# Kernel optimization log

Hardware: AMD Instinct MI355X
Metric: run time of the kernel (lower is better)

Reference implementation:

```python
import jax, jax.numpy as jnp
import numpy as np

B, C, N = 8, 512, 4096
G = 8          # GroupNorm groups (8 <= C)
EPS = 1e-6


def setup_inputs() -> dict:
    key = jax.random.key(0)
    ks = jax.random.split(key, 5)
    return {
        "x": jax.random.normal(ks[0], (B, C, N), dtype=jnp.float32),
        "qkv_w": jax.random.normal(ks[1], (3 * C, C), dtype=jnp.float32) * (C ** -0.5),
        "qkv_b": jax.random.normal(ks[2], (3 * C,), dtype=jnp.float32) * 0.02,
        "proj_w": jax.random.normal(ks[3], (C, C), dtype=jnp.float32) * (C ** -0.5),
        "proj_b": jax.random.normal(ks[4], (C,), dtype=jnp.float32) * 0.02,
        "gn_scale": jnp.ones((C,), dtype=jnp.float32),
        "gn_bias": jnp.zeros((C,), dtype=jnp.float32),
    }


def group_norm(x, scale, bias):
    b, c, n = x.shape
    xr = x.reshape(b, G, c // G, n)
    mean = xr.mean(axis=(2, 3), keepdims=True)
    var = xr.var(axis=(2, 3), keepdims=True)
    h = ((xr - mean) * jax.lax.rsqrt(var + EPS)).reshape(b, c, n)
    return h * scale[None, :, None] + bias[None, :, None]


def reference(x, qkv_w, qkv_b, proj_w, proj_b, gn_scale, gn_bias):
    c = x.shape[1]
    h = group_norm(x, gn_scale, gn_bias)
    # 1x1 Conv1d == channel-mixing GEMM
    qkv = jnp.einsum('oc,bcn->bon', qkv_w, h) + qkv_b[None, :, None]
    q, k, v = jnp.split(qkv, 3, axis=1)           # each [B, C, N]
    q = q * (c ** -0.5)
    k = jax.nn.softmax(k, axis=-1)                # softmax over tokens
    # linear attention: context = k v^T over tokens, then project q
    context = jnp.einsum('bdn,ben->bde', k, v)    # [B, C, C]
    out = jnp.einsum('bde,bdn->ben', context, q)  # [B, C, N]
    y = jnp.einsum('oc,bcn->bon', proj_w, out) + proj_b[None, :, None]
    return x + y
```

## Files before the change

kernel.cpp:

```cpp
#include <hip/hip_runtime.h>

#define BB 8
#define CC 512
#define NT 4096
#define GG 8
#define CPG 64
#define EPSF 1e-6f
#define SQK 0.04419417382415922f

typedef __attribute__((ext_vector_type(8))) short bf16x8;
typedef __attribute__((ext_vector_type(4))) float f32x4;

#define OFF_RED  0
#define OFF_PB2  4096
#define OFF_IZ   270336
#define OFF_WKV  274432
#define OFF_PWB  536576
#define OFF_WQT  667648
#define OFF_MB   798720
#define OFF_PBF  1847296
#define OFF_CTXB 2895872
#define OFF_PCTX 3944448
#define OFF_HT   12333056
#define OFF_KVB  20721664

__device__ __forceinline__ ushort f2bf(float f) {
  union { float f; uint u; } v; v.f = f;
  uint r = (v.u + 0x7fffu + ((v.u >> 16) & 1u)) >> 16;
  return (ushort)r;
}
__device__ __forceinline__ float bf2f(ushort h) {
  union { uint u; float f; } v; v.u = ((uint)h) << 16;
  return v.f;
}
__device__ __forceinline__ uint pk(float a, float b) {
  return (uint)f2bf(a) | ((uint)f2bf(b) << 16);
}
__device__ __forceinline__ void gload16(const ushort* g, ushort* l) {
  __builtin_amdgcn_global_load_lds((const __attribute__((address_space(1))) void*)g,
                                   (__attribute__((address_space(3))) void*)l, 16, 0, 0);
}
#define KSWZ(kofs, row) ((kofs) ^ ((((row) >> 1) & 3) << 3))

__global__ __launch_bounds__(256) void gn_stats1(const float* __restrict__ x,
                                                 float* __restrict__ red) {
  int bg = blockIdx.y, chunk = blockIdx.x;
  const float4* p4 = (const float4*)(x + (size_t)bg * (CPG * NT) + (size_t)chunk * 32768);
  int tid = threadIdx.x;
  float s = 0.f, sq = 0.f;
  for (int i = tid; i < 8192; i += 256) {
    float4 v = p4[i];
    s  += v.x + v.y + v.z + v.w;
    sq += v.x * v.x + v.y * v.y + v.z * v.z + v.w * v.w;
  }
  for (int off = 32; off > 0; off >>= 1) {
    s  += __shfl_down(s, off);
    sq += __shfl_down(sq, off);
  }
  __shared__ float ls[4], lq[4];
  int wid = tid >> 6, lane = tid & 63;
  if (lane == 0) { ls[wid] = s; lq[wid] = sq; }
  __syncthreads();
  if (tid == 0) {
    red[(bg * 8 + chunk) * 2]     = ls[0] + ls[1] + ls[2] + ls[3];
    red[(bg * 8 + chunk) * 2 + 1] = lq[0] + lq[1] + lq[2] + lq[3];
  }
}

__global__ __launch_bounds__(256) void wconv2(const float* __restrict__ qkv_w,
                                              const float* __restrict__ proj_w,
                                              ushort* __restrict__ wkvb,
                                              ushort* __restrict__ pwb) {
  int bid = blockIdx.x;
  if (bid < 512) {
    int idx = (bid * 256 + threadIdx.x) * 4;
    float4 v = *(const float4*)(qkv_w + (size_t)CC * CC + idx);
    *(uint2*)(wkvb + idx) = make_uint2(pk(v.x, v.y), pk(v.z, v.w));
  } else {
    int idx = ((bid - 512) * 256 + threadIdx.x) * 4;
    float4 v = *(const float4*)(proj_w + idx);
    *(uint2*)(pwb + idx) = make_uint2(pk(v.x, v.y), pk(v.z, v.w));
  }
}

__global__ __launch_bounds__(256) void wqt_kernel(const float* __restrict__ qkv_w,
                                                  ushort* __restrict__ wqT) {
  __shared__ float t[32][33];
  int d0 = blockIdx.y * 32, c0 = blockIdx.x * 32;
  int tid = threadIdx.x;
  int r = tid >> 3, c4 = (tid & 7) * 4;
  float4 v = *(const float4*)(qkv_w + (size_t)(d0 + r) * CC + c0 + c4);
  t[r][c4] = v.x; t[r][c4 + 1] = v.y; t[r][c4 + 2] = v.z; t[r][c4 + 3] = v.w;
  __syncthreads();
  int r2 = tid >> 3, d4 = (tid & 7) * 4;
  uint w0 = pk(t[d4][r2], t[d4 + 1][r2]);
  uint w1 = pk(t[d4 + 2][r2], t[d4 + 3][r2]);
  *(uint2*)&wqT[(size_t)(c0 + r2) * CC + d0 + d4] = make_uint2(w0, w1);
}

__global__ __launch_bounds__(256) void ht_kernel(
    const float* __restrict__ x, const float* __restrict__ red,
    const float* __restrict__ gn_scale, const float* __restrict__ gn_bias,
    ushort* __restrict__ hT) {
  __shared__ float ts[64][68];
  __shared__ float la[64], lb[64];
  int b = blockIdx.z, g = blockIdx.y, n0 = blockIdx.x * 64;
  int c0 = g * 64;
  int tid = threadIdx.x;
  if (tid == 0) {
    int bg = b * 8 + g;
    float s = 0.f, sq = 0.f;
#pragma unroll
    for (int i = 0; i < 8; i++) {
      s  += red[(bg * 8 + i) * 2];
      sq += red[(bg * 8 + i) * 2 + 1];
    }
    float mean = s / (float)(CPG * NT);
    float var  = sq / (float)(CPG * NT) - mean * mean;
    ts[0][0] = mean; ts[0][1] = rsqrtf(var + EPSF);
  }
  __syncthreads();
  if (tid < 64) {
    float mean = ts[0][0], rstd = ts[0][1];
    float a = gn_scale[c0 + tid] * rstd;
    la[tid] = a;
    lb[tid] = gn_bias[c0 + tid] - mean * a;
  }
  __syncthreads();
  int tn = (tid & 15) * 4, tc = tid >> 4;
#pragma unroll
  for (int it = 0; it < 4; it++) {
    int c = tc + it * 16;
    float a  = la[c];
    float bb = lb[c];
    float4 v = *(const float4*)(x + ((size_t)(b * CC + c0 + c)) * NT + n0 + tn);
    ts[c][tn]     = a * v.x + bb;
    ts[c][tn + 1] = a * v.y + bb;
    ts[c][tn + 2] = a * v.z + bb;
    ts[c][tn + 3] = a * v.w + bb;
  }
  __syncthreads();
#pragma unroll
  for (int it = 0; it < 2; it++) {
    int idx = tid + it * 256;
    int n = idx >> 3, c8 = (idx & 7) * 8;
    uint w[4];
#pragma unroll
    for (int j = 0; j < 4; j++)
      w[j] = pk(ts[c8 + 2 * j][n], ts[c8 + 2 * j + 1][n]);
    *(uint4*)&hT[((size_t)b * NT + n0 + n) * CC + c0 + c8] = make_uint4(w[0], w[1], w[2], w[3]);
  }
}

template <int KTOT, int LDA, int LDB>
__device__ __forceinline__ void mfma_loop(const ushort* __restrict__ A,
                                          const ushort* __restrict__ B,
                                          ushort* As, ushort* Bs, int tid,
                                          f32x4 acc[4][4]) {
  int wave = tid >> 6, lane = tid & 63;
  int srow = lane >> 2;
  int kofs = KSWZ((lane & 3) * 8, srow);
  int r0 = wave * 16 + srow;
  int r1 = (wave + 4) * 16 + srow;
  const ushort* ga0 = A + (size_t)r0 * LDA + kofs;
  const ushort* ga1 = A + (size_t)r1 * LDA + kofs;
  const ushort* gb0 = B + (size_t)r0 * LDB + kofs;
  const ushort* gb1 = B + (size_t)r1 * LDB + kofs;
  int lo0 = wave * 512, lo1 = (wave + 4) * 512;
  int wm = (wave >> 1) * 64, wn = (wave & 1) * 64;
  int rowl = lane & 15;
  int kread = KSWZ((lane >> 4) * 8, rowl);
  int aoff = (wm + rowl) * 32 + kread;
  int boff = (wn + rowl) * 32 + kread;
  constexpr int NIT = KTOT / 32;
  gload16(ga0, As + lo0); gload16(ga1, As + lo1);
  gload16(gb0, Bs + lo0); gload16(gb1, Bs + lo1);
  ga0 += 32; ga1 += 32; gb0 += 32; gb1 += 32;
#pragma unroll 1
  for (int t = 0; t < NIT; t++) {
    int cb = (t & 1) * 4096;
    int nb = 4096 - cb;
    if (t + 1 < NIT) {
      gload16(ga0, As + nb + lo0); gload16(ga1, As + nb + lo1);
      gload16(gb0, Bs + nb + lo0); gload16(gb1, Bs + nb + lo1);
      ga0 += 32; ga1 += 32; gb0 += 32; gb1 += 32;
      asm volatile("s_waitcnt vmcnt(4)" ::: "memory");
    } else {
      asm volatile("s_waitcnt vmcnt(0)" ::: "memory");
    }
    __builtin_amdgcn_s_barrier();
    asm volatile("" ::: "memory");
    bf16x8 a[4], b[4];
#pragma unroll
    for (int m = 0; m < 4; m++) a[m] = *(const bf16x8*)(As + cb + aoff + m * 512);
#pragma unroll
    for (int n = 0; n < 4; n++) b[n] = *(const bf16x8*)(Bs + cb + boff + n * 512);
#pragma unroll
    for (int m = 0; m < 4; m++)
#pragma unroll
      for (int n = 0; n < 4; n++)
        acc[m][n] = __builtin_amdgcn_mfma_f32_16x16x32_bf16(a[m], b[n], acc[m][n], 0, 0, 0);
    asm volatile("" ::: "memory");
    __builtin_amdgcn_s_barrier();
    asm volatile("" ::: "memory");
  }
}

template <int KTOT, int LDA, int LDB>
__device__ __forceinline__ void mfma_loop64(const ushort* __restrict__ A,
                                            const ushort* __restrict__ B,
                                            ushort* As, ushort* Bs, int tid,
                                            f32x4 acc[2][2]) {
  int wave = tid >> 6, lane = tid & 63;
  int srow = tid >> 2;
  int kofs = KSWZ((tid & 3) * 8, srow & 15);
  const ushort* ga = A + (size_t)srow * LDA + kofs;
  const ushort* gb = B + (size_t)srow * LDB + kofs;
  int lo = wave * 512;
  int wm = (wave >> 1) * 32, wn = (wave & 1) * 32;
  int rowl = lane & 15;
  int kread = KSWZ((lane >> 4) * 8, rowl);
  int aoff = (wm + rowl) * 32 + kread;
  int boff = (wn + rowl) * 32 + kread;
  constexpr int NIT = KTOT / 32;
  gload16(ga, As + lo); gload16(gb, Bs + lo);
  ga += 32; gb += 32;
#pragma unroll 1
  for (int t = 0; t < NIT; t++) {
    int cb = (t & 1) * 2048;
    int nb = 2048 - cb;
    if (t + 1 < NIT) {
      gload16(ga, As + nb + lo); gload16(gb, Bs + nb + lo);
      ga += 32; gb += 32;
      asm volatile("s_waitcnt vmcnt(2)" ::: "memory");
    } else {
      asm volatile("s_waitcnt vmcnt(0)" ::: "memory");
    }
    __builtin_amdgcn_s_barrier();
    asm volatile("" ::: "memory");
    bf16x8 a[2], b[2];
#pragma unroll
    for (int m = 0; m < 2; m++) a[m] = *(const bf16x8*)(As + cb + aoff + m * 512);
#pragma unroll
    for (int n = 0; n < 2; n++) b[n] = *(const bf16x8*)(Bs + cb + boff + n * 512);
#pragma unroll
    for (int m = 0; m < 2; m++)
#pragma unroll
      for (int n = 0; n < 2; n++)
        acc[m][n] = __builtin_amdgcn_mfma_f32_16x16x32_bf16(a[m], b[n], acc[m][n], 0, 0, 0);
    asm volatile("" ::: "memory");
    __builtin_amdgcn_s_barrier();
    asm volatile("" ::: "memory");
  }
}

__global__ __launch_bounds__(256) void kv_gemm_bf16(
    const ushort* __restrict__ wkvb, const ushort* __restrict__ hT,
    const float* __restrict__ qkv_b, ushort* __restrict__ kvb) {
  __shared__ ushort As[8192], Bs[8192];
  int b = blockIdx.z, n0 = blockIdx.x * 128, m0 = blockIdx.y * 128;
  int tid = threadIdx.x;
  f32x4 acc[4][4] = {{{0.f, 0.f, 0.f, 0.f}}};
  mfma_loop<CC, CC, CC>(wkvb + (size_t)m0 * CC,
                        hT + (size_t)b * NT * CC + (size_t)n0 * CC, As, Bs, tid, acc);
  int wave = tid >> 6, lane = tid & 63;
  int wm = (wave >> 1) * 64, wn = (wave & 1) * 64;
  int col = lane & 15, rb = (lane >> 4) * 4;
  bool isK = (m0 < 512);
#pragma unroll
  for (int m = 0; m < 4; m++)
#pragma unroll
    for (int n = 0; n < 4; n++)
#pragma unroll
      for (int j = 0; j < 4; j++) {
        int gm = m0 + wm + m * 16 + rb + j;
        int gn = n0 + wn + n * 16 + col;
        float val = acc[m][n][j] + qkv_b[CC + gm];
        if (isK) val = __expf(val);
        kvb[((size_t)(b * 1024 + gm)) * NT + gn] = f2bf(val);
      }
}

__global__ __launch_bounds__(256) void zred(const ushort* __restrict__ kvb,
                                            float* __restrict__ invZ) {
  int row = blockIdx.x;
  int b = row >> 9, d = row & 511;
  const ushort* p = kvb + ((size_t)(b * 1024 + d)) * NT;
  int tid = threadIdx.x;
  uint4 r0 = *(const uint4*)(p + tid * 16);
  uint4 r1 = *(const uint4*)(p + tid * 16 + 8);
  uint w[8] = {r0.x, r0.y, r0.z, r0.w, r1.x, r1.y, r1.z, r1.w};
  float s = 0.f;
#pragma unroll
  for (int i = 0; i < 8; i++) {
    union { uint u; float f; } lo, hi;
    lo.u = w[i] << 16; hi.u = w[i] & 0xffff0000u;
    s += lo.f + hi.f;
  }
  for (int off = 32; off > 0; off >>= 1) s += __shfl_down(s, off);
  __shared__ float red[4];
  int wid = tid >> 6, lane = tid & 63;
  if (lane == 0) red[wid] = s;
  __syncthreads();
  if (tid == 0) invZ[row] = 1.f / (red[0] + red[1] + red[2] + red[3]);
}

__global__ __launch_bounds__(256) void ctx_gemm_split(
    const ushort* __restrict__ kvb, ushort* __restrict__ pctx) {
  __shared__ ushort As[8192], Bs[8192];
  int e0 = blockIdx.x * 128, d0 = blockIdx.y * 128;
  int bz = blockIdx.z, b = bz >> 3, s = bz & 7;
  int tid = threadIdx.x;
  f32x4 acc[4][4] = {{{0.f, 0.f, 0.f, 0.f}}};
  const ushort* K = kvb + (size_t)b * 1024 * NT + (size_t)d0 * NT + s * 512;
  const ushort* V = kvb + ((size_t)b * 1024 + 512) * NT + (size_t)e0 * NT + s * 512;
  mfma_loop<512, NT, NT>(K, V, As, Bs, tid, acc);
  int wave = tid >> 6, lane = tid & 63;
  int wm = (wave >> 1) * 64, wn = (wave & 1) * 64;
  int col = lane & 15, rb = (lane >> 4) * 4;
#pragma unroll
  for (int m = 0; m < 4; m++)
#pragma unroll
    for (int n = 0; n < 4; n++)
#pragma unroll
      for (int j = 0; j < 4; j++) {
        int gd = d0 + wm + m * 16 + rb + j;
        int ge = e0 + wn + n * 16 + col;
        pctx[((size_t)(b * 8 + s) * CC + gd) * CC + ge] = f2bf(acc[m][n][j]);
      }
}

__global__ __launch_bounds__(256) void ctx_red(const ushort* __restrict__ pctx,
                                               const float* __restrict__ invZ,
                                               ushort* __restrict__ ctxb) {
  int t = blockIdx.x * 256 + threadIdx.x;
  int b = t >> 15;
  int r = (t & 32767) * 8;
  int d = r >> 9;
  float iz = invZ[b * 512 + d];
  const ushort* base = pctx + (size_t)b * 8 * 262144 + r;
  float f[8] = {};
#pragma unroll
  for (int s = 0; s < 8; s++) {
    uint4 v = *(const uint4*)(base + (size_t)s * 262144);
    uint w[4] = {v.x, v.y, v.z, v.w};
#pragma unroll
    for (int j = 0; j < 4; j++) {
      union { uint u; float f; } lo, hi;
      lo.u = w[j] << 16; hi.u = w[j] & 0xffff0000u;
      f[2 * j] += lo.f; f[2 * j + 1] += hi.f;
    }
  }
  uint o[4];
#pragma unroll
  for (int j = 0; j < 4; j++) o[j] = pk(f[2 * j] * iz, f[2 * j + 1] * iz);
  *(uint4*)(ctxb + (size_t)b * 262144 + r) = make_uint4(o[0], o[1], o[2], o[3]);
}

__global__ __launch_bounds__(256) void m_gemm_bf16(
    const ushort* __restrict__ pwb, const ushort* __restrict__ ctxb,
    ushort* __restrict__ Mb) {
  __shared__ ushort As[4096], Bs[4096];
  int b = blockIdx.z, d0 = blockIdx.x * 64, o0 = blockIdx.y * 64;
  int tid = threadIdx.x;
  f32x4 acc[2][2] = {{{0.f, 0.f, 0.f, 0.f}}};
  mfma_loop64<CC, CC, CC>(pwb + (size_t)o0 * CC,
                          ctxb + (size_t)b * CC * CC + (size_t)d0 * CC, As, Bs, tid, acc);
  int wave = tid >> 6, lane = tid & 63;
  int wm = (wave >> 1) * 32, wn = (wave & 1) * 32;
  int col = lane & 15, rb = (lane >> 4) * 4;
#pragma unroll
  for (int m = 0; m < 2; m++)
#pragma unroll
    for (int n = 0; n < 2; n++)
#pragma unroll
      for (int j = 0; j < 4; j++) {
        int go = o0 + wm + m * 16 + rb + j;
        int gd = d0 + wn + n * 16 + col;
        Mb[((size_t)b * CC + go) * CC + gd] = f2bf(acc[m][n][j] * SQK);
      }
}

__global__ __launch_bounds__(256) void p_gemm_bf16(
    const ushort* __restrict__ Mb, const ushort* __restrict__ wqT,
    ushort* __restrict__ Pb) {
  __shared__ ushort As[4096], Bs[4096];
  int b = blockIdx.z, c0 = blockIdx.x * 64, o0 = blockIdx.y * 64;
  int tid = threadIdx.x;
  f32x4 acc[2][2] = {{{0.f, 0.f, 0.f, 0.f}}};
  mfma_loop64<CC, CC, CC>(Mb + (size_t)b * CC * CC + (size_t)o0 * CC,
                          wqT + (size_t)c0 * CC, As, Bs, tid, acc);
  int wave = tid >> 6, lane = tid & 63;
  int wm = (wave >> 1) * 32, wn = (wave & 1) * 32;
  int col = lane & 15, rb = (lane >> 4) * 4;
#pragma unroll
  for (int m = 0; m < 2; m++)
#pragma unroll
    for (int n = 0; n < 2; n++)
#pragma unroll
      for (int j = 0; j < 4; j++) {
        int go = o0 + wm + m * 16 + rb + j;
        int gc = c0 + wn + n * 16 + col;
        Pb[((size_t)b * CC + go) * CC + gc] = f2bf(acc[m][n][j]);
      }
}

__global__ __launch_bounds__(256) void pb2_kernel(
    const ushort* __restrict__ Mb, const float* __restrict__ qkv_b,
    const float* __restrict__ proj_b, float* __restrict__ pb2) {
  int b = blockIdx.x, og = blockIdx.y;
  int r = og * 64 + (threadIdx.x >> 2);
  int q = threadIdx.x & 3;
  const ushort* Mr = Mb + ((size_t)(b * CC + r)) * CC + q * 128;
  const float* bq = qkv_b + q * 128;
  float s = 0.f;
#pragma unroll
  for (int i = 0; i < 16; i++) {
    uint4 v = *(const uint4*)(Mr + i * 8);
    uint w[4] = {v.x, v.y, v.z, v.w};
#pragma unroll
    for (int j = 0; j < 4; j++) {
      union { uint u; float f; } lo, hi;
      lo.u = w[j] << 16; hi.u = w[j] & 0xffff0000u;
      s += lo.f * bq[i * 8 + 2 * j] + hi.f * bq[i * 8 + 2 * j + 1];
    }
  }
  s += __shfl_xor(s, 1);
  s += __shfl_xor(s, 2);
  if (q == 0) pb2[b * CC + r] = s + proj_b[r];
}

__global__ __launch_bounds__(256) void final_gemm_bf16(
    const float* __restrict__ x, const ushort* __restrict__ Pb,
    const ushort* __restrict__ hT, const float* __restrict__ pb2,
    float* __restrict__ out) {
  __shared__ ushort As[8192], Bs[8192];
  int b = blockIdx.z, n0 = blockIdx.x * 128, m0 = blockIdx.y * 128;
  int tid = threadIdx.x;
  f32x4 acc[4][4] = {{{0.f, 0.f, 0.f, 0.f}}};
  mfma_loop<CC, CC, CC>(Pb + (size_t)b * CC * CC + (size_t)m0 * CC,
                        hT + (size_t)b * NT * CC + (size_t)n0 * CC, As, Bs, tid, acc);
  int wave = tid >> 6, lane = tid & 63;
  int wm = (wave >> 1) * 64, wn = (wave & 1) * 64;
  int col = lane & 15, rb = (lane >> 4) * 4;
#pragma unroll
  for (int m = 0; m < 4; m++)
#pragma unroll
    for (int n = 0; n < 4; n++)
#pragma unroll
      for (int j = 0; j < 4; j++) {
        int gm = m0 + wm + m * 16 + rb + j;
        int gn = n0 + wn + n * 16 + col;
        size_t idx = ((size_t)(b * CC + gm)) * NT + gn;
        out[idx] = acc[m][n][j] + pb2[b * CC + gm] + x[idx];
      }
}

extern "C" void kernel_launch(void* const* d_in, const int* in_sizes, int n_in,
                              void* d_out, int out_size, void* d_ws, size_t ws_size,
                              hipStream_t stream) {
  const float* x        = (const float*)d_in[0];
  const float* qkv_w    = (const float*)d_in[1];
  const float* qkv_b    = (const float*)d_in[2];
  const float* proj_w   = (const float*)d_in[3];
  const float* proj_b   = (const float*)d_in[4];
  const float* gn_scale = (const float*)d_in[5];
  const float* gn_bias  = (const float*)d_in[6];
  float* out = (float*)d_out;
  float* ws  = (float*)d_ws;

  float*  red   = ws + OFF_RED;
  float*  pb2   = ws + OFF_PB2;
  float*  invZ  = ws + OFF_IZ;
  ushort* wkvb  = (ushort*)(ws + OFF_WKV);
  ushort* pwb   = (ushort*)(ws + OFF_PWB);
  ushort* wqT   = (ushort*)(ws + OFF_WQT);
  ushort* Mb    = (ushort*)(ws + OFF_MB);
  ushort* Pb    = (ushort*)(ws + OFF_PBF);
  ushort* ctxb  = (ushort*)(ws + OFF_CTXB);
  ushort* pctx  = (ushort*)(ws + OFF_PCTX);
  ushort* hT    = (ushort*)(ws + OFF_HT);
  ushort* kvb   = (ushort*)(ws + OFF_KVB);

  gn_stats1<<<dim3(8, 64), 256, 0, stream>>>(x, red);
  wconv2<<<768, 256, 0, stream>>>(qkv_w, proj_w, wkvb, pwb);
  wqt_kernel<<<dim3(16, 16), 256, 0, stream>>>(qkv_w, wqT);
  ht_kernel<<<dim3(64, 8, 8), 256, 0, stream>>>(x, red, gn_scale, gn_bias, hT);
  kv_gemm_bf16<<<dim3(32, 8, 8), 256, 0, stream>>>(wkvb, hT, qkv_b, kvb);
  zred<<<4096, 256, 0, stream>>>(kvb, invZ);
  ctx_gemm_split<<<dim3(4, 4, 64), 256, 0, stream>>>(kvb, pctx);
  ctx_red<<<1024, 256, 0, stream>>>(pctx, invZ, ctxb);
  m_gemm_bf16<<<dim3(8, 8, 8), 256, 0, stream>>>(pwb, ctxb, Mb);
  p_gemm_bf16<<<dim3(8, 8, 8), 256, 0, stream>>>(Mb, wqT, Pb);
  pb2_kernel<<<dim3(8, 8), 256, 0, stream>>>(Mb, qkv_b, proj_b, pb2);
  final_gemm_bf16<<<dim3(32, 4, 8), 256, 0, stream>>>(x, Pb, hT, pb2, out);
}
```

Measured before the change: 208.4 us.

## Enlarge big GEMM tiles to 256x256 with 512 threads and K=64 stages

```diff
diff --git a/kernel.cpp b/kernel.cpp
--- a/kernel.cpp
+++ b/kernel.cpp
@@ -152,57 +152,68 @@
   }
 }
 
-template <int KTOT, int LDA, int LDB>
-__device__ __forceinline__ void mfma_loop(const ushort* __restrict__ A,
-                                          const ushort* __restrict__ B,
-                                          ushort* As, ushort* Bs, int tid,
-                                          f32x4 acc[4][4]) {
-  int wave = tid >> 6, lane = tid & 63;
-  int srow = lane >> 2;
-  int kofs = KSWZ((lane & 3) * 8, srow);
-  int r0 = wave * 16 + srow;
-  int r1 = (wave + 4) * 16 + srow;
-  const ushort* ga0 = A + (size_t)r0 * LDA + kofs;
-  const ushort* ga1 = A + (size_t)r1 * LDA + kofs;
-  const ushort* gb0 = B + (size_t)r0 * LDB + kofs;
-  const ushort* gb1 = B + (size_t)r1 * LDB + kofs;
-  int lo0 = wave * 512, lo1 = (wave + 4) * 512;
-  int wm = (wave >> 1) * 64, wn = (wave & 1) * 64;
-  int rowl = lane & 15;
-  int kread = KSWZ((lane >> 4) * 8, rowl);
-  int aoff = (wm + rowl) * 32 + kread;
-  int boff = (wn + rowl) * 32 + kread;
-  constexpr int NIT = KTOT / 32;
-  gload16(ga0, As + lo0); gload16(ga1, As + lo1);
-  gload16(gb0, Bs + lo0); gload16(gb1, Bs + lo1);
-  ga0 += 32; ga1 += 32; gb0 += 32; gb1 += 32;
+#define TBUF 16384
+
+__device__ __forceinline__ void stage256(const ushort* __restrict__ G, ushort* L,
+                                         int LD, int wave, int lane) {
+  int rw = wave * 8 + (lane >> 3);
+  int cg = lane & 7;
+#pragma unroll
+  for (int s = 0; s < 4; s++) {
+    int row = s * 64 + rw;
+    int gcol = (cg ^ (row & 7)) * 8;
+    gload16(G + (size_t)row * LD + gcol, L + s * 4096 + wave * 512);
+  }
+}
+
+template <int NTILES>
+__device__ __forceinline__ void mfma256(const ushort* __restrict__ A,
+                                        const ushort* __restrict__ B,
+                                        int LDA, int LDB, ushort* As, ushort* Bs,
+                                        int tid, f32x4 acc[8][4]) {
+  int wave = tid >> 6, lane = tid & 63;
+  int wr = wave >> 2, wc = wave & 3;
+  stage256(A, As, LDA, wave, lane);
+  stage256(B, Bs, LDB, wave, lane);
+  const ushort* gA = A + 64;
+  const ushort* gB = B + 64;
+  int rowA = wr * 128 + (lane & 15);
+  int rowB = wc * 64 + (lane & 15);
+  int kg0 = lane >> 4;
 #pragma unroll 1
-  for (int t = 0; t < NIT; t++) {
-    int cb = (t & 1) * 4096;
-    int nb = 4096 - cb;
-    if (t + 1 < NIT) {
-      gload16(ga0, As + nb + lo0); gload16(ga1, As + nb + lo1);
-      gload16(gb0, Bs + nb + lo0); gload16(gb1, Bs + nb + lo1);
-      ga0 += 32; ga1 += 32; gb0 += 32; gb1 += 32;
-      asm volatile("s_waitcnt vmcnt(4)" ::: "memory");
+  for (int t = 0; t < NTILES; t++) {
+    __builtin_amdgcn_s_barrier();
+    asm volatile("" ::: "memory");
+    if (t + 1 < NTILES) {
+      stage256(gA, As + ((t + 1) & 1) * TBUF, LDA, wave, lane);
+      stage256(gB, Bs + ((t + 1) & 1) * TBUF, LDB, wave, lane);
+      gA += 64; gB += 64;
+      asm volatile("s_waitcnt vmcnt(8)" ::: "memory");
     } else {
       asm volatile("s_waitcnt vmcnt(0)" ::: "memory");
     }
     __builtin_amdgcn_s_barrier();
     asm volatile("" ::: "memory");
-    bf16x8 a[4], b[4];
-#pragma unroll
-    for (int m = 0; m < 4; m++) a[m] = *(const bf16x8*)(As + cb + aoff + m * 512);
-#pragma unroll
-    for (int n = 0; n < 4; n++) b[n] = *(const bf16x8*)(Bs + cb + boff + n * 512);
-#pragma unroll
-    for (int m = 0; m < 4; m++)
-#pragma unroll
-      for (int n = 0; n < 4; n++)
-        acc[m][n] = __builtin_amdgcn_mfma_f32_16x16x32_bf16(a[m], b[n], acc[m][n], 0, 0, 0);
-    asm volatile("" ::: "memory");
-    __builtin_amdgcn_s_barrier();
-    asm volatile("" ::: "memory");
+    const ushort* Ab = As + (t & 1) * TBUF;
+    const ushort* Bb = Bs + (t & 1) * TBUF;
+#pragma unroll
+    for (int kk = 0; kk < 2; kk++) {
+      int kg = kg0 + kk * 4;
+      bf16x8 bfr[4];
+#pragma unroll
+      for (int ni = 0; ni < 4; ni++) {
+        int r = rowB + ni * 16;
+        bfr[ni] = *(const bf16x8*)(Bb + r * 64 + ((kg ^ (r & 7)) << 3));
+      }
+#pragma unroll
+      for (int mi = 0; mi < 8; mi++) {
+        int r = rowA + mi * 16;
+        bf16x8 afr = *(const bf16x8*)(Ab + r * 64 + ((kg ^ (r & 7)) << 3));
+#pragma unroll
+        for (int ni = 0; ni < 4; ni++)
+          acc[mi][ni] = __builtin_amdgcn_mfma_f32_16x16x32_bf16(afr, bfr[ni], acc[mi][ni], 0, 0, 0);
+      }
+    }
   }
 }
 
@@ -254,31 +265,35 @@
   }
 }
 
-__global__ __launch_bounds__(256) void kv_gemm_bf16(
+__global__ __launch_bounds__(512) void kv_gemm_bf16(
     const ushort* __restrict__ wkvb, const ushort* __restrict__ hT,
     const float* __restrict__ qkv_b, ushort* __restrict__ kvb) {
-  __shared__ ushort As[8192], Bs[8192];
-  int b = blockIdx.z, n0 = blockIdx.x * 128, m0 = blockIdx.y * 128;
-  int tid = threadIdx.x;
-  f32x4 acc[4][4] = {{{0.f, 0.f, 0.f, 0.f}}};
-  mfma_loop<CC, CC, CC>(wkvb + (size_t)m0 * CC,
-                        hT + (size_t)b * NT * CC + (size_t)n0 * CC, As, Bs, tid, acc);
-  int wave = tid >> 6, lane = tid & 63;
-  int wm = (wave >> 1) * 64, wn = (wave & 1) * 64;
+  extern __shared__ ushort lds[];
+  ushort* As = lds;
+  ushort* Bs = lds + 2 * TBUF;
+  int b = blockIdx.z, n0 = blockIdx.x * 256, m0 = blockIdx.y * 256;
+  int tid = threadIdx.x;
+  f32x4 acc[8][4] = {{{0.f, 0.f, 0.f, 0.f}}};
+  mfma256<8>(wkvb + (size_t)m0 * CC, hT + (size_t)b * NT * CC + (size_t)n0 * CC,
+             CC, CC, As, Bs, tid, acc);
+  int wave = tid >> 6, lane = tid & 63;
+  int wr = wave >> 2, wc = wave & 3;
   int col = lane & 15, rb = (lane >> 4) * 4;
   bool isK = (m0 < 512);
 #pragma unroll
-  for (int m = 0; m < 4; m++)
-#pragma unroll
-    for (int n = 0; n < 4; n++)
-#pragma unroll
-      for (int j = 0; j < 4; j++) {
-        int gm = m0 + wm + m * 16 + rb + j;
-        int gn = n0 + wn + n * 16 + col;
-        float val = acc[m][n][j] + qkv_b[CC + gm];
+  for (int mi = 0; mi < 8; mi++)
+#pragma unroll
+    for (int j = 0; j < 4; j++) {
+      int gm = m0 + wr * 128 + mi * 16 + rb + j;
+      float bias = qkv_b[CC + gm];
+      ushort* orow = kvb + ((size_t)(b * 1024 + gm)) * NT + n0 + wc * 64 + col;
+#pragma unroll
+      for (int ni = 0; ni < 4; ni++) {
+        float val = acc[mi][ni][j] + bias;
         if (isK) val = __expf(val);
-        kvb[((size_t)(b * 1024 + gm)) * NT + gn] = f2bf(val);
+        orow[ni * 16] = f2bf(val);
       }
+    }
 }
 
 __global__ __launch_bounds__(256) void zred(const ushort* __restrict__ kvb,
@@ -305,29 +320,31 @@
   if (tid == 0) invZ[row] = 1.f / (red[0] + red[1] + red[2] + red[3]);
 }
 
-__global__ __launch_bounds__(256) void ctx_gemm_split(
+__global__ __launch_bounds__(512) void ctx_gemm_split(
     const ushort* __restrict__ kvb, ushort* __restrict__ pctx) {
-  __shared__ ushort As[8192], Bs[8192];
-  int e0 = blockIdx.x * 128, d0 = blockIdx.y * 128;
+  extern __shared__ ushort lds[];
+  ushort* As = lds;
+  ushort* Bs = lds + 2 * TBUF;
+  int e0 = blockIdx.x * 256, d0 = blockIdx.y * 256;
   int bz = blockIdx.z, b = bz >> 3, s = bz & 7;
   int tid = threadIdx.x;
-  f32x4 acc[4][4] = {{{0.f, 0.f, 0.f, 0.f}}};
+  f32x4 acc[8][4] = {{{0.f, 0.f, 0.f, 0.f}}};
   const ushort* K = kvb + (size_t)b * 1024 * NT + (size_t)d0 * NT + s * 512;
   const ushort* V = kvb + ((size_t)b * 1024 + 512) * NT + (size_t)e0 * NT + s * 512;
-  mfma_loop<512, NT, NT>(K, V, As, Bs, tid, acc);
-  int wave = tid >> 6, lane = tid & 63;
-  int wm = (wave >> 1) * 64, wn = (wave & 1) * 64;
+  mfma256<8>(K, V, NT, NT, As, Bs, tid, acc);
+  int wave = tid >> 6, lane = tid & 63;
+  int wr = wave >> 2, wc = wave & 3;
   int col = lane & 15, rb = (lane >> 4) * 4;
 #pragma unroll
-  for (int m = 0; m < 4; m++)
-#pragma unroll
-    for (int n = 0; n < 4; n++)
-#pragma unroll
-      for (int j = 0; j < 4; j++) {
-        int gd = d0 + wm + m * 16 + rb + j;
-        int ge = e0 + wn + n * 16 + col;
-        pctx[((size_t)(b * 8 + s) * CC + gd) * CC + ge] = f2bf(acc[m][n][j]);
-      }
+  for (int mi = 0; mi < 8; mi++)
+#pragma unroll
+    for (int j = 0; j < 4; j++) {
+      int gd = d0 + wr * 128 + mi * 16 + rb + j;
+      ushort* orow = pctx + ((size_t)(b * 8 + s) * CC + gd) * CC + e0 + wc * 64 + col;
+#pragma unroll
+      for (int ni = 0; ni < 4; ni++)
+        orow[ni * 16] = f2bf(acc[mi][ni][j]);
+    }
 }
 
 __global__ __launch_bounds__(256) void ctx_red(const ushort* __restrict__ pctx,
@@ -430,30 +447,32 @@
   if (q == 0) pb2[b * CC + r] = s + proj_b[r];
 }
 
-__global__ __launch_bounds__(256) void final_gemm_bf16(
+__global__ __launch_bounds__(512) void final_gemm_bf16(
     const float* __restrict__ x, const ushort* __restrict__ Pb,
     const ushort* __restrict__ hT, const float* __restrict__ pb2,
     float* __restrict__ out) {
-  __shared__ ushort As[8192], Bs[8192];
-  int b = blockIdx.z, n0 = blockIdx.x * 128, m0 = blockIdx.y * 128;
-  int tid = threadIdx.x;
-  f32x4 acc[4][4] = {{{0.f, 0.f, 0.f, 0.f}}};
-  mfma_loop<CC, CC, CC>(Pb + (size_t)b * CC * CC + (size_t)m0 * CC,
-                        hT + (size_t)b * NT * CC + (size_t)n0 * CC, As, Bs, tid, acc);
-  int wave = tid >> 6, lane = tid & 63;
-  int wm = (wave >> 1) * 64, wn = (wave & 1) * 64;
+  extern __shared__ ushort lds[];
+  ushort* As = lds;
+  ushort* Bs = lds + 2 * TBUF;
+  int b = blockIdx.z, n0 = blockIdx.x * 256, m0 = blockIdx.y * 256;
+  int tid = threadIdx.x;
+  f32x4 acc[8][4] = {{{0.f, 0.f, 0.f, 0.f}}};
+  mfma256<8>(Pb + (size_t)b * CC * CC + (size_t)m0 * CC,
+             hT + (size_t)b * NT * CC + (size_t)n0 * CC, CC, CC, As, Bs, tid, acc);
+  int wave = tid >> 6, lane = tid & 63;
+  int wr = wave >> 2, wc = wave & 3;
   int col = lane & 15, rb = (lane >> 4) * 4;
 #pragma unroll
-  for (int m = 0; m < 4; m++)
-#pragma unroll
-    for (int n = 0; n < 4; n++)
-#pragma unroll
-      for (int j = 0; j < 4; j++) {
-        int gm = m0 + wm + m * 16 + rb + j;
-        int gn = n0 + wn + n * 16 + col;
-        size_t idx = ((size_t)(b * CC + gm)) * NT + gn;
-        out[idx] = acc[m][n][j] + pb2[b * CC + gm] + x[idx];
-      }
+  for (int mi = 0; mi < 8; mi++)
+#pragma unroll
+    for (int j = 0; j < 4; j++) {
+      int gm = m0 + wr * 128 + mi * 16 + rb + j;
+      float bias = pb2[b * CC + gm];
+      size_t rowoff = ((size_t)(b * CC + gm)) * NT + n0 + wc * 64 + col;
+#pragma unroll
+      for (int ni = 0; ni < 4; ni++)
+        out[rowoff + ni * 16] = acc[mi][ni][j] + bias + x[rowoff + ni * 16];
+    }
 }
 
 extern "C" void kernel_launch(void* const* d_in, const int* in_sizes, int n_in,
@@ -482,16 +501,26 @@
   ushort* hT    = (ushort*)(ws + OFF_HT);
   ushort* kvb   = (ushort*)(ws + OFF_KVB);
 
+  constexpr int DSM = 4 * TBUF * 2;
+  static bool attr_set = false;
+  (void)attr_set;
+  hipFuncSetAttribute((const void*)kv_gemm_bf16,
+                      hipFuncAttributeMaxDynamicSharedMemorySize, DSM);
+  hipFuncSetAttribute((const void*)ctx_gemm_split,
+                      hipFuncAttributeMaxDynamicSharedMemorySize, DSM);
+  hipFuncSetAttribute((const void*)final_gemm_bf16,
+                      hipFuncAttributeMaxDynamicSharedMemorySize, DSM);
+
   gn_stats1<<<dim3(8, 64), 256, 0, stream>>>(x, red);
   wconv2<<<768, 256, 0, stream>>>(qkv_w, proj_w, wkvb, pwb);
   wqt_kernel<<<dim3(16, 16), 256, 0, stream>>>(qkv_w, wqT);
   ht_kernel<<<dim3(64, 8, 8), 256, 0, stream>>>(x, red, gn_scale, gn_bias, hT);
-  kv_gemm_bf16<<<dim3(32, 8, 8), 256, 0, stream>>>(wkvb, hT, qkv_b, kvb);
+  kv_gemm_bf16<<<dim3(16, 4, 8), 512, DSM, stream>>>(wkvb, hT, qkv_b, kvb);
   zred<<<4096, 256, 0, stream>>>(kvb, invZ);
-  ctx_gemm_split<<<dim3(4, 4, 64), 256, 0, stream>>>(kvb, pctx);
+  ctx_gemm_split<<<dim3(2, 2, 64), 512, DSM, stream>>>(kvb, pctx);
   ctx_red<<<1024, 256, 0, stream>>>(pctx, invZ, ctxb);
   m_gemm_bf16<<<dim3(8, 8, 8), 256, 0, stream>>>(pwb, ctxb, Mb);
   p_gemm_bf16<<<dim3(8, 8, 8), 256, 0, stream>>>(Mb, wqT, Pb);
   pb2_kernel<<<dim3(8, 8), 256, 0, stream>>>(Mb, qkv_b, proj_b, pb2);
-  final_gemm_bf16<<<dim3(32, 4, 8), 256, 0, stream>>>(x, Pb, hT, pb2, out);
-}
+  final_gemm_bf16<<<dim3(16, 2, 8), 512, DSM, stream>>>(x, Pb, hT, pb2, out);
+}
```

Result: faster. 194.6 us (-6.6%).
